# Kernel tuning notes

Measured on AMD Instinct MI355X. Metric: run time of the kernel, lower is better.

## Reference

```python
import jax, jax.numpy as jnp
import numpy as np

# Default widths from CWT.__init__: round((exp(linspace(0,2.5,5))-1)*30)+1
WIDTHS = [1, 27, 76, 167, 336]


def _morlet_int_psi():
    """pywt 'morl' wavelet: psi(t)=exp(-t^2/2)*cos(5t) on [-8,8], precision=10,
    integrated (cumulative) as in pywt.integrate_wavelet."""
    precision = 10
    n = 2 ** precision
    lb, ub = -8.0, 8.0
    t = np.linspace(lb, ub, n)
    psi = np.exp(-t ** 2 / 2.0) * np.cos(5.0 * t)
    step = t[1] - t[0]
    int_psi = np.cumsum(psi) * step
    return int_psi, step, lb, ub, n


def _filters(widths):
    """Per-scale resampled integrated wavelet, as in pywt.cwt.
    pywt uses np.convolve(data, int_psi[j][::-1]) (which flips its kernel);
    lax conv is a correlation (no flip), so the equivalent lax kernel is int_psi[j]."""
    int_psi, step, lb, ub, n = _morlet_int_psi()
    filts = []
    for scale in widths:
        j = (np.arange(scale * (ub - lb) + 1) / (scale * step)).astype(np.int64)
        j = j[j < n]
        filts.append(int_psi[j].astype(np.float32))
    return filts

_FILTERS = _filters(WIDTHS)


def _cwt_forward(x):
    # x: [N, T, C]; conv along T, channels independent
    N, T, C = x.shape
    xt = x.transpose(0, 2, 1).reshape(N * C, 1, T)  # [N*C, 1, T]
    outs = []
    for scale, f in zip(WIDTHS, _FILTERS):
        L = f.shape[0]
        k = jnp.asarray(f)[None, None, :]  # [out=1, in=1, L]
        # 'full' convolution: pad L-1 on each side
        conv = jax.lax.conv_general_dilated(xt, k, window_strides=(1,), padding=[(L - 1, L - 1)])  # [N*C,1,T+L-1]
        coef = (-np.sqrt(float(scale))) * jnp.diff(conv, axis=-1)  # [N*C,1,T+L-2]
        d = (coef.shape[-1] - T) / 2.0  # trim to central T samples (pywt)
        lo = int(np.floor(d))
        hi = coef.shape[-1] - int(np.ceil(d))
        coef = coef[..., lo:hi]  # [N*C, 1, T]
        outs.append(coef.reshape(N, C, T))
    out = jnp.stack(outs, axis=0)  # [F, N, C, T]
    return out.transpose(1, 3, 2, 0)  # [N, T, C, F]


def setup_inputs() -> dict:
    key = jax.random.key(0)
    x = jax.random.normal(key, (16, 2048, 64), dtype=jnp.float32)
    return {"x": x}


def reference(x):
    return _cwt_forward(x)
```

## Files before the change

kernel.cpp:

```cpp
#include <hip/hip_runtime.h>
#include <hip/hip_fp16.h>
#include <math.h>

#define NB    16
#define T     2048
#define NC    64
#define NROWS (NB*NC)
#define PADL2 2696
#define XSH_N 7440

#define WTOT_U4 19840

#define WS_XT    (1u<<19)
#define WS_OUTT  ((1u<<19) + (1u<<22))

typedef _Float16 half8  __attribute__((ext_vector_type(8)));
typedef _Float16 half4v __attribute__((ext_vector_type(4)));
typedef float    f32x4  __attribute__((ext_vector_type(4)));

__global__ __launch_bounds__(1024) void cwt_prep(const float* __restrict__ x,
                                                 __half* __restrict__ xT,
                                                 __half* __restrict__ W) {
    __shared__ double ps[1024];
    __shared__ double sc[1024];
    __shared__ float  k32[1024];
    __shared__ float  tile4[4][64 * 65];
    const int tid = threadIdx.x;

    if (blockIdx.x == 0) {
        uint4* W4 = (uint4*)W;
        const uint4 z = make_uint4(0u, 0u, 0u, 0u);
        for (int i = tid; i < WTOT_U4; i += 1024) W4[i] = z;

        const double delta = 16.0 / 1023.0;
        double t = (tid == 1023) ? 8.0 : (-8.0 + delta * (double)tid);
        ps[tid] = exp(-0.5 * t * t) * cos(5.0 * t);
        __syncthreads();

        double* a = ps; double* b = sc;
        for (int off = 1; off < 1024; off <<= 1) {
            double v = a[tid];
            if (tid >= off) v += a[tid - off];
            b[tid] = v;
            __syncthreads();
            double* tmp = a; a = b; b = tmp;
        }
        const double step = ((-8.0 + delta) + 8.0);
        k32[tid] = (float)(a[tid] * step);
        __syncthreads();

        constexpr int SCe[5]   = {336, 167, 76, 27, 1};
        constexpr int KS2[5]   = {5408, 2720, 1248, 480, 64};
        constexpr int WOFFe[5] = {0, 86528, 130048, 150016, 157696};
        constexpr int CLOe[5]  = {0, 42, 65, 77, 83};
        for (int sl = 0; sl < 5; ++sl) {
            const int s = SCe[sl];
            const int L = 16 * s + 1;
            const double c = (double)s * step;
            const float sq = (float)sqrt((double)s);
            const int posoff = PADL2 - 8 * s - 1;
            const int kb0 = posoff - 32 * CLOe[sl];
            __half* wb = W + WOFFe[sl];
            const int Ks = KS2[sl];
            for (int i = tid; i <= L; i += 1024) {
                float g; bool wr = true;
                if (i == 0) {
                    g = sq * k32[0];
                } else if (i == L) {
                    long long jl = (long long)((double)(L - 1) / c);
                    if (jl > 1023) jl = 1023;
                    g = -sq * k32[jl];
                } else {
                    long long j1 = (long long)((double)i / c);
                    long long j0 = (long long)((double)(i - 1) / c);
                    if (j1 > 1023) j1 = 1023;
                    if (j0 > 1023) j0 = 1023;
                    wr = (j1 > j0);
                    g = sq * (k32[j1] - k32[j0]);
                }
                if (wr) {
                    const __half hg = __float2half(g);
                    const int kb = kb0 + i;
                    #pragma unroll
                    for (int bb = 0; bb < 16; ++bb)
                        wb[bb * Ks + kb + bb] = hg;
                }
            }
        }
    } else {
        const int g    = tid >> 8;
        const int t256 = tid & 255;
        const int ti   = (blockIdx.x - 1) * 4 + g;
        const int n    = ti >> 5;
        const int t0   = (ti & 31) << 6;
        float* tl = tile4[g];

        const float4* src = (const float4*)(x + ((size_t)(n * T + t0)) * NC);
        #pragma unroll
        for (int k = 0; k < 4; ++k) {
            float4 v = src[t256 + 256 * k];
            const int flat = (t256 + 256 * k) * 4;
            const int tt = flat >> 6, c = flat & 63;
            tl[tt * 65 + c + 0] = v.x;
            tl[tt * 65 + c + 1] = v.y;
            tl[tt * 65 + c + 2] = v.z;
            tl[tt * 65 + c + 3] = v.w;
        }
        __syncthreads();
        const int lane = t256 & 63, w4 = t256 >> 6;
        for (int cc = w4; cc < 64; cc += 4) {
            xT[((size_t)(n * 64 + cc)) * T + t0 + lane] = __float2half(tl[lane * 65 + cc]);
        }
    }
}

template<int N, int DEPTH>
__device__ __forceinline__ void conv_seg(int c0, int c1,
                                         const _Float16* __restrict__ xb,
                                         const _Float16* const (&ap)[5],
                                         f32x4 (&acc)[5][4]) {
    half8 A[DEPTH][N];
    half8 B[DEPTH][4];
    #pragma unroll
    for (int d = 0; d < DEPTH; ++d) {
        const int ko = (c0 + d) << 5;
        #pragma unroll
        for (int sl = 0; sl < N; ++sl) A[d][sl] = *(const half8*)(ap[sl] + ko);
        #pragma unroll
        for (int j = 0; j < 4; ++j)   B[d][j]  = *(const half8*)(xb + 256 * j + ko);
    }
    int c = c0;
    for (; c + DEPTH <= c1; c += DEPTH) {
        #pragma unroll
        for (int d = 0; d < DEPTH; ++d) {
            #pragma unroll
            for (int sl = 0; sl < N; ++sl) {
                acc[sl][0] = __builtin_amdgcn_mfma_f32_16x16x32_f16(A[d][sl], B[d][0], acc[sl][0], 0, 0, 0);
                acc[sl][1] = __builtin_amdgcn_mfma_f32_16x16x32_f16(A[d][sl], B[d][1], acc[sl][1], 0, 0, 0);
                acc[sl][2] = __builtin_amdgcn_mfma_f32_16x16x32_f16(A[d][sl], B[d][2], acc[sl][2], 0, 0, 0);
                acc[sl][3] = __builtin_amdgcn_mfma_f32_16x16x32_f16(A[d][sl], B[d][3], acc[sl][3], 0, 0, 0);
            }
            const int ko = (c + DEPTH + d) << 5;
            #pragma unroll
            for (int sl = 0; sl < N; ++sl) A[d][sl] = *(const half8*)(ap[sl] + ko);
            #pragma unroll
            for (int j = 0; j < 4; ++j)   B[d][j]  = *(const half8*)(xb + 256 * j + ko);
        }
    }
    #pragma unroll
    for (int d = 0; d < DEPTH; ++d) {
        if (d < c1 - c) {
            #pragma unroll
            for (int sl = 0; sl < N; ++sl) {
                acc[sl][0] = __builtin_amdgcn_mfma_f32_16x16x32_f16(A[d][sl], B[d][0], acc[sl][0], 0, 0, 0);
                acc[sl][1] = __builtin_amdgcn_mfma_f32_16x16x32_f16(A[d][sl], B[d][1], acc[sl][1], 0, 0, 0);
                acc[sl][2] = __builtin_amdgcn_mfma_f32_16x16x32_f16(A[d][sl], B[d][2], acc[sl][2], 0, 0, 0);
                acc[sl][3] = __builtin_amdgcn_mfma_f32_16x16x32_f16(A[d][sl], B[d][3], acc[sl][3], 0, 0, 0);
            }
        }
    }
}

__global__ __launch_bounds__(128, 2) void cwt_conv_mfma(const __half* __restrict__ xT,
                                                        const __half* __restrict__ Wg,
                                                        __half* __restrict__ outT) {
    constexpr int KS2[5]   = {5408, 2720, 1248, 480, 64};
    constexpr int WOFFe[5] = {0, 86528, 130048, 150016, 157696};
    constexpr int CLOe[5]  = {0, 42, 65, 77, 83};
    constexpr int OS[5]    = {4, 3, 2, 1, 0};

    __shared__ _Float16 xsh[XSH_N];
    __shared__ _Float16 ostage[2048];
    const int tid  = threadIdx.x;
    const int row  = blockIdx.x;
    const int nidx = row >> 6;
    const int cidx = row & 63;
    const int lane = tid & 63;
    const int w    = tid >> 6;
    const int mcol = lane & 15;
    const int grp  = lane >> 4;

    {
        uint4* x4 = (uint4*)xsh;
        const uint4 z = make_uint4(0u, 0u, 0u, 0u);
        for (int i = tid; i < XSH_N / 8; i += 128)
            if (i < PADL2 / 8 || i >= (PADL2 + T) / 8) x4[i] = z;
        const uint4* src = (const uint4*)(xT + (size_t)row * T);
        x4[PADL2 / 8 + tid] = src[tid];
        x4[PADL2 / 8 + 128 + tid] = src[128 + tid];
    }
    __syncthreads();

    const _Float16* xb = xsh + 1024 * w + 16 * mcol + 8 * grp;
    const _Float16* ap[5];
    #pragma unroll
    for (int sl = 0; sl < 5; ++sl)
        ap[sl] = (const _Float16*)Wg + WOFFe[sl] + mcol * KS2[sl] + 8 * grp
                 - (CLOe[sl] << 5);

    f32x4 acc[5][4];
    #pragma unroll
    for (int sl = 0; sl < 5; ++sl)
        #pragma unroll
        for (int j = 0; j < 4; ++j)
            acc[sl][j] = (f32x4){0.f, 0.f, 0.f, 0.f};

    conv_seg<1,3>(  0,  42, xb, ap, acc);
    conv_seg<2,3>( 42,  65, xb, ap, acc);
    conv_seg<3,2>( 65,  77, xb, ap, acc);
    conv_seg<4,2>( 77,  83, xb, ap, acc);
    conv_seg<5,2>( 83,  85, xb, ap, acc);
    conv_seg<4,2>( 85,  92, xb, ap, acc);
    conv_seg<3,2>( 92, 104, xb, ap, acc);
    conv_seg<2,3>(104, 127, xb, ap, acc);
    conv_seg<1,3>(127, 169, xb, ap, acc);

    _Float16* os = ostage + 1024 * w;
    #pragma unroll
    for (int sl = 0; sl < 5; ++sl) {
        #pragma unroll
        for (int j = 0; j < 4; ++j) {
            half4v h;
            #pragma unroll
            for (int r = 0; r < 4; ++r) h[r] = (_Float16)acc[sl][j][r];
            *(half4v*)(os + 256 * j + 16 * mcol + 4 * grp) = h;
        }
        half8 o0 = *(const half8*)(os + 16 * lane);
        half8 o1 = *(const half8*)(os + 16 * lane + 8);
        __half* ob = outT + ((size_t)(((nidx * 128 + 64 * w + lane) * 64 + cidx) * 5 + OS[sl])) * 16;
        *(half8*)(ob)     = o0;
        *(half8*)(ob + 8) = o1;
    }
}

__global__ __launch_bounds__(256) void cwt_fix(const __half* __restrict__ outT,
                                               float* __restrict__ out) {
    __shared__ float tile[16 * 320];
    const int b  = blockIdx.x;
    const int n  = b >> 7;
    const int tb = b & 127;
    const int tid = threadIdx.x;

    const uint4* src = (const uint4*)(outT + (size_t)(n * 128 + tb) * 5120);
    for (int i = tid; i < 640; i += 256) {
        uint4 v = src[i];
        const __half* h = (const __half*)&v;
        const int h0  = i * 8;
        const int sg  = h0 >> 4;
        const int tt0 = h0 & 15;
        #pragma unroll
        for (int k = 0; k < 8; ++k) tile[(tt0 + k) * 320 + sg] = __half2float(h[k]);
    }
    __syncthreads();
    float4* dst = (float4*)(out + (size_t)(n * 2048 + tb * 16) * 320);
    const float4* tl = (const float4*)tile;
    for (int k = tid; k < 1280; k += 256) dst[k] = tl[k];
}

extern "C" void kernel_launch(void* const* d_in, const int* in_sizes, int n_in,
                              void* d_out, int out_size, void* d_ws, size_t ws_size,
                              hipStream_t stream) {
    const float* x = (const float*)d_in[0];
    float* out = (float*)d_out;
    char* ws = (char*)d_ws;

    __half* W    = (__half*)ws;
    __half* xT   = (__half*)(ws + WS_XT);
    __half* outT = (__half*)(ws + WS_OUTT);

    cwt_prep<<<129, 1024, 0, stream>>>(x, xT, W);
    cwt_conv_mfma<<<NROWS, 128, 0, stream>>>(xT, W, outT);
    cwt_fix<<<2048, 256, 0, stream>>>(outT, out);
}
```

Baseline: 144.0 us.

## Split conv reduction across wave pairs and parallelize filter build over 16 blocks

The MFMA conv kernel now runs 4 waves per block instead of 2. Each pair of waves handles half of the K-segment range for the same output tile, and the partial accumulators are reduced through shared memory before the write-out. The prep kernel's single filter-building block becomes 16 blocks, one per diagonal shift, each zeroing and writing its own slice of the Toeplitz weight matrix. The goal is more parallelism and latency hiding in the conv and less serial work in prep, at the cost of extra LDS usage, two reduction barriers and redundant cumsum work in each prep block.

```diff
diff --git a/kernel.cpp b/kernel.cpp
--- a/kernel.cpp
+++ b/kernel.cpp
@@ -9,7 +9,6 @@
 #define PADL2 2696
 #define XSH_N 7440
 
-#define WTOT_U4 19840
 
 #define WS_XT    (1u<<19)
 #define WS_OUTT  ((1u<<19) + (1u<<22))
@@ -27,10 +26,22 @@
     __shared__ float  tile4[4][64 * 65];
     const int tid = threadIdx.x;
 
-    if (blockIdx.x == 0) {
-        uint4* W4 = (uint4*)W;
-        const uint4 z = make_uint4(0u, 0u, 0u, 0u);
-        for (int i = tid; i < WTOT_U4; i += 1024) W4[i] = z;
+    if (blockIdx.x < 16) {
+        const int bb = blockIdx.x;
+        constexpr int SCe[5]   = {336, 167, 76, 27, 1};
+        constexpr int KS2[5]   = {5408, 2720, 1248, 480, 64};
+        constexpr int WOFFe[5] = {0, 86528, 130048, 150016, 157696};
+        constexpr int CLOe[5]  = {0, 42, 65, 77, 83};
+
+        {
+            const uint4 z = make_uint4(0u, 0u, 0u, 0u);
+            #pragma unroll
+            for (int sl = 0; sl < 5; ++sl) {
+                uint4* z4 = (uint4*)(W + WOFFe[sl] + bb * KS2[sl]);
+                const int n8 = KS2[sl] / 8;
+                for (int i = tid; i < n8; i += 1024) z4[i] = z;
+            }
+        }
 
         const double delta = 16.0 / 1023.0;
         double t = (tid == 1023) ? 8.0 : (-8.0 + delta * (double)tid);
@@ -49,10 +60,6 @@
         k32[tid] = (float)(a[tid] * step);
         __syncthreads();
 
-        constexpr int SCe[5]   = {336, 167, 76, 27, 1};
-        constexpr int KS2[5]   = {5408, 2720, 1248, 480, 64};
-        constexpr int WOFFe[5] = {0, 86528, 130048, 150016, 157696};
-        constexpr int CLOe[5]  = {0, 42, 65, 77, 83};
         for (int sl = 0; sl < 5; ++sl) {
             const int s = SCe[sl];
             const int L = 16 * s + 1;
@@ -79,18 +86,14 @@
                     g = sq * (k32[j1] - k32[j0]);
                 }
                 if (wr) {
-                    const __half hg = __float2half(g);
-                    const int kb = kb0 + i;
-                    #pragma unroll
-                    for (int bb = 0; bb < 16; ++bb)
-                        wb[bb * Ks + kb + bb] = hg;
+                    wb[bb * Ks + kb0 + i + bb] = __float2half(g);
                 }
             }
         }
     } else {
         const int g    = tid >> 8;
         const int t256 = tid & 255;
-        const int ti   = (blockIdx.x - 1) * 4 + g;
+        const int ti   = (blockIdx.x - 16) * 4 + g;
         const int n    = ti >> 5;
         const int t0   = (ti & 31) << 6;
         float* tl = tile4[g];
@@ -161,7 +164,7 @@
     }
 }
 
-__global__ __launch_bounds__(128, 2) void cwt_conv_mfma(const __half* __restrict__ xT,
+__global__ __launch_bounds__(256, 4) void cwt_conv_mfma(const __half* __restrict__ xT,
                                                         const __half* __restrict__ Wg,
                                                         __half* __restrict__ outT) {
     constexpr int KS2[5]   = {5408, 2720, 1248, 480, 64};
@@ -171,27 +174,29 @@
 
     __shared__ _Float16 xsh[XSH_N];
     __shared__ _Float16 ostage[2048];
+    __shared__ float    red[2][2][1088];
     const int tid  = threadIdx.x;
     const int row  = blockIdx.x;
     const int nidx = row >> 6;
     const int cidx = row & 63;
     const int lane = tid & 63;
     const int w    = tid >> 6;
+    const int wh   = w & 1;
+    const int wp   = w >> 1;
     const int mcol = lane & 15;
     const int grp  = lane >> 4;
 
     {
         uint4* x4 = (uint4*)xsh;
         const uint4 z = make_uint4(0u, 0u, 0u, 0u);
-        for (int i = tid; i < XSH_N / 8; i += 128)
+        for (int i = tid; i < XSH_N / 8; i += 256)
             if (i < PADL2 / 8 || i >= (PADL2 + T) / 8) x4[i] = z;
         const uint4* src = (const uint4*)(xT + (size_t)row * T);
         x4[PADL2 / 8 + tid] = src[tid];
-        x4[PADL2 / 8 + 128 + tid] = src[128 + tid];
     }
     __syncthreads();
 
-    const _Float16* xb = xsh + 1024 * w + 16 * mcol + 8 * grp;
+    const _Float16* xb = xsh + 1024 * wh + 16 * mcol + 8 * grp;
     const _Float16* ap[5];
     #pragma unroll
     for (int sl = 0; sl < 5; ++sl)
@@ -205,31 +210,61 @@
         for (int j = 0; j < 4; ++j)
             acc[sl][j] = (f32x4){0.f, 0.f, 0.f, 0.f};
 
-    conv_seg<1,3>(  0,  42, xb, ap, acc);
-    conv_seg<2,3>( 42,  65, xb, ap, acc);
-    conv_seg<3,2>( 65,  77, xb, ap, acc);
-    conv_seg<4,2>( 77,  83, xb, ap, acc);
-    conv_seg<5,2>( 83,  85, xb, ap, acc);
-    conv_seg<4,2>( 85,  92, xb, ap, acc);
-    conv_seg<3,2>( 92, 104, xb, ap, acc);
-    conv_seg<2,3>(104, 127, xb, ap, acc);
-    conv_seg<1,3>(127, 169, xb, ap, acc);
-
-    _Float16* os = ostage + 1024 * w;
-    #pragma unroll
-    for (int sl = 0; sl < 5; ++sl) {
-        #pragma unroll
-        for (int j = 0; j < 4; ++j) {
-            half4v h;
-            #pragma unroll
-            for (int r = 0; r < 4; ++r) h[r] = (_Float16)acc[sl][j][r];
-            *(half4v*)(os + 256 * j + 16 * mcol + 4 * grp) = h;
-        }
-        half8 o0 = *(const half8*)(os + 16 * lane);
-        half8 o1 = *(const half8*)(os + 16 * lane + 8);
-        __half* ob = outT + ((size_t)(((nidx * 128 + 64 * w + lane) * 64 + cidx) * 5 + OS[sl])) * 16;
-        *(half8*)(ob)     = o0;
-        *(half8*)(ob + 8) = o1;
+    if (wp == 0) {
+        conv_seg<1,3>(  0,  42, xb, ap, acc);
+        conv_seg<2,3>( 42,  65, xb, ap, acc);
+        conv_seg<3,2>( 65,  77, xb, ap, acc);
+        conv_seg<4,2>( 77,  83, xb, ap, acc);
+        conv_seg<5,2>( 83,  85, xb, ap, acc);
+    } else {
+        conv_seg<4,2>( 85,  92, xb, ap, acc);
+        conv_seg<3,2>( 92, 104, xb, ap, acc);
+        conv_seg<2,3>(104, 127, xb, ap, acc);
+        conv_seg<1,3>(127, 169, xb, ap, acc);
+    }
+
+    #pragma unroll
+    for (int rnd = 0; rnd < 2; ++rnd) {
+        const int s0 = rnd * 2;
+        if (wp == 1) {
+            #pragma unroll
+            for (int s = 0; s < 2; ++s)
+                #pragma unroll
+                for (int j = 0; j < 4; ++j)
+                    #pragma unroll
+                    for (int r = 0; r < 4; ++r)
+                        red[s][wh][lane * 17 + j * 4 + r] = acc[s0 + s][j][r];
+        }
+        __syncthreads();
+        if (wp == 0) {
+            #pragma unroll
+            for (int s = 0; s < 2; ++s)
+                #pragma unroll
+                for (int j = 0; j < 4; ++j)
+                    #pragma unroll
+                    for (int r = 0; r < 4; ++r)
+                        acc[s0 + s][j][r] += red[s][wh][lane * 17 + j * 4 + r];
+        }
+        __syncthreads();
+    }
+
+    if (wp == 0) {
+        _Float16* os = ostage + 1024 * wh;
+        #pragma unroll
+        for (int sl = 0; sl < 5; ++sl) {
+            #pragma unroll
+            for (int j = 0; j < 4; ++j) {
+                half4v h;
+                #pragma unroll
+                for (int r = 0; r < 4; ++r) h[r] = (_Float16)acc[sl][j][r];
+                *(half4v*)(os + 256 * j + 16 * mcol + 4 * grp) = h;
+            }
+            half8 o0 = *(const half8*)(os + 16 * lane);
+            half8 o1 = *(const half8*)(os + 16 * lane + 8);
+            __half* ob = outT + ((size_t)(((nidx * 128 + 64 * wh + lane) * 64 + cidx) * 5 + OS[sl])) * 16;
+            *(half8*)(ob)     = o0;
+            *(half8*)(ob + 8) = o1;
+        }
     }
 }
 
@@ -268,7 +303,7 @@
     __half* xT   = (__half*)(ws + WS_XT);
     __half* outT = (__half*)(ws + WS_OUTT);
 
-    cwt_prep<<<129, 1024, 0, stream>>>(x, xT, W);
-    cwt_conv_mfma<<<NROWS, 128, 0, stream>>>(xT, W, outT);
+    cwt_prep<<<144, 1024, 0, stream>>>(x, xT, W);
+    cwt_conv_mfma<<<NROWS, 256, 0, stream>>>(xT, W, outT);
     cwt_fix<<<2048, 256, 0, stream>>>(outT, out);
 }
```

Measured after the change: 210.9 us. 1.46x slower.

## Split conv rows across two blocks and parallelize filter build over 16 blocks

Applied to the files above, without the earlier changes.

The convolution kernel now launches two blocks per signal row. Each block computes half the time tiles, with accumulators halved from [5][4] to [5][2] and launch bounds raised to 4 blocks per SM, which gives more parallelism and occupancy. Each block still loads the full row into shared memory, so the shared staging work is duplicated. The prep kernel spreads zeroing and filter construction over 16 blocks (one per diagonal shift) instead of one, at the cost of recomputing the wavelet prefix scan in each block.

```diff
diff --git a/kernel.cpp b/kernel.cpp
--- a/kernel.cpp
+++ b/kernel.cpp
@@ -9,7 +9,6 @@
 #define PADL2 2696
 #define XSH_N 7440
 
-#define WTOT_U4 19840
 
 #define WS_XT    (1u<<19)
 #define WS_OUTT  ((1u<<19) + (1u<<22))
@@ -27,10 +26,22 @@
     __shared__ float  tile4[4][64 * 65];
     const int tid = threadIdx.x;
 
-    if (blockIdx.x == 0) {
-        uint4* W4 = (uint4*)W;
-        const uint4 z = make_uint4(0u, 0u, 0u, 0u);
-        for (int i = tid; i < WTOT_U4; i += 1024) W4[i] = z;
+    if (blockIdx.x < 16) {
+        const int bb = blockIdx.x;
+        constexpr int SCe[5]   = {336, 167, 76, 27, 1};
+        constexpr int KS2[5]   = {5408, 2720, 1248, 480, 64};
+        constexpr int WOFFe[5] = {0, 86528, 130048, 150016, 157696};
+        constexpr int CLOe[5]  = {0, 42, 65, 77, 83};
+
+        {
+            const uint4 z = make_uint4(0u, 0u, 0u, 0u);
+            #pragma unroll
+            for (int sl = 0; sl < 5; ++sl) {
+                uint4* z4 = (uint4*)(W + WOFFe[sl] + bb * KS2[sl]);
+                const int n8 = KS2[sl] / 8;
+                for (int i = tid; i < n8; i += 1024) z4[i] = z;
+            }
+        }
 
         const double delta = 16.0 / 1023.0;
         double t = (tid == 1023) ? 8.0 : (-8.0 + delta * (double)tid);
@@ -49,10 +60,6 @@
         k32[tid] = (float)(a[tid] * step);
         __syncthreads();
 
-        constexpr int SCe[5]   = {336, 167, 76, 27, 1};
-        constexpr int KS2[5]   = {5408, 2720, 1248, 480, 64};
-        constexpr int WOFFe[5] = {0, 86528, 130048, 150016, 157696};
-        constexpr int CLOe[5]  = {0, 42, 65, 77, 83};
         for (int sl = 0; sl < 5; ++sl) {
             const int s = SCe[sl];
             const int L = 16 * s + 1;
@@ -79,18 +86,14 @@
                     g = sq * (k32[j1] - k32[j0]);
                 }
                 if (wr) {
-                    const __half hg = __float2half(g);
-                    const int kb = kb0 + i;
-                    #pragma unroll
-                    for (int bb = 0; bb < 16; ++bb)
-                        wb[bb * Ks + kb + bb] = hg;
+                    wb[bb * Ks + kb0 + i + bb] = __float2half(g);
                 }
             }
         }
     } else {
         const int g    = tid >> 8;
         const int t256 = tid & 255;
-        const int ti   = (blockIdx.x - 1) * 4 + g;
+        const int ti   = (blockIdx.x - 16) * 4 + g;
         const int n    = ti >> 5;
         const int t0   = (ti & 31) << 6;
         float* tl = tile4[g];
@@ -118,16 +121,16 @@
 __device__ __forceinline__ void conv_seg(int c0, int c1,
                                          const _Float16* __restrict__ xb,
                                          const _Float16* const (&ap)[5],
-                                         f32x4 (&acc)[5][4]) {
+                                         f32x4 (&acc)[5][2]) {
     half8 A[DEPTH][N];
-    half8 B[DEPTH][4];
+    half8 B[DEPTH][2];
     #pragma unroll
     for (int d = 0; d < DEPTH; ++d) {
         const int ko = (c0 + d) << 5;
         #pragma unroll
         for (int sl = 0; sl < N; ++sl) A[d][sl] = *(const half8*)(ap[sl] + ko);
         #pragma unroll
-        for (int j = 0; j < 4; ++j)   B[d][j]  = *(const half8*)(xb + 256 * j + ko);
+        for (int j = 0; j < 2; ++j)   B[d][j]  = *(const half8*)(xb + 256 * j + ko);
     }
     int c = c0;
     for (; c + DEPTH <= c1; c += DEPTH) {
@@ -137,14 +140,12 @@
             for (int sl = 0; sl < N; ++sl) {
                 acc[sl][0] = __builtin_amdgcn_mfma_f32_16x16x32_f16(A[d][sl], B[d][0], acc[sl][0], 0, 0, 0);
                 acc[sl][1] = __builtin_amdgcn_mfma_f32_16x16x32_f16(A[d][sl], B[d][1], acc[sl][1], 0, 0, 0);
-                acc[sl][2] = __builtin_amdgcn_mfma_f32_16x16x32_f16(A[d][sl], B[d][2], acc[sl][2], 0, 0, 0);
-                acc[sl][3] = __builtin_amdgcn_mfma_f32_16x16x32_f16(A[d][sl], B[d][3], acc[sl][3], 0, 0, 0);
             }
             const int ko = (c + DEPTH + d) << 5;
             #pragma unroll
             for (int sl = 0; sl < N; ++sl) A[d][sl] = *(const half8*)(ap[sl] + ko);
             #pragma unroll
-            for (int j = 0; j < 4; ++j)   B[d][j]  = *(const half8*)(xb + 256 * j + ko);
+            for (int j = 0; j < 2; ++j)   B[d][j]  = *(const half8*)(xb + 256 * j + ko);
         }
     }
     #pragma unroll
@@ -154,14 +155,12 @@
             for (int sl = 0; sl < N; ++sl) {
                 acc[sl][0] = __builtin_amdgcn_mfma_f32_16x16x32_f16(A[d][sl], B[d][0], acc[sl][0], 0, 0, 0);
                 acc[sl][1] = __builtin_amdgcn_mfma_f32_16x16x32_f16(A[d][sl], B[d][1], acc[sl][1], 0, 0, 0);
-                acc[sl][2] = __builtin_amdgcn_mfma_f32_16x16x32_f16(A[d][sl], B[d][2], acc[sl][2], 0, 0, 0);
-                acc[sl][3] = __builtin_amdgcn_mfma_f32_16x16x32_f16(A[d][sl], B[d][3], acc[sl][3], 0, 0, 0);
-            }
-        }
-    }
-}
-
-__global__ __launch_bounds__(128, 2) void cwt_conv_mfma(const __half* __restrict__ xT,
+            }
+        }
+    }
+}
+
+__global__ __launch_bounds__(128, 4) void cwt_conv_mfma(const __half* __restrict__ xT,
                                                         const __half* __restrict__ Wg,
                                                         __half* __restrict__ outT) {
     constexpr int KS2[5]   = {5408, 2720, 1248, 480, 64};
@@ -170,9 +169,11 @@
     constexpr int OS[5]    = {4, 3, 2, 1, 0};
 
     __shared__ _Float16 xsh[XSH_N];
-    __shared__ _Float16 ostage[2048];
+    __shared__ _Float16 ostage[1024];
     const int tid  = threadIdx.x;
-    const int row  = blockIdx.x;
+    const int bid  = blockIdx.x;
+    const int row  = bid >> 1;
+    const int h    = bid & 1;
     const int nidx = row >> 6;
     const int cidx = row & 63;
     const int lane = tid & 63;
@@ -191,18 +192,19 @@
     }
     __syncthreads();
 
-    const _Float16* xb = xsh + 1024 * w + 16 * mcol + 8 * grp;
+    const int g0 = 64 * h + 32 * w;
+    const _Float16* xb = xsh + 16 * g0 + 16 * mcol + 8 * grp;
     const _Float16* ap[5];
     #pragma unroll
     for (int sl = 0; sl < 5; ++sl)
         ap[sl] = (const _Float16*)Wg + WOFFe[sl] + mcol * KS2[sl] + 8 * grp
                  - (CLOe[sl] << 5);
 
-    f32x4 acc[5][4];
+    f32x4 acc[5][2];
     #pragma unroll
     for (int sl = 0; sl < 5; ++sl)
         #pragma unroll
-        for (int j = 0; j < 4; ++j)
+        for (int j = 0; j < 2; ++j)
             acc[sl][j] = (f32x4){0.f, 0.f, 0.f, 0.f};
 
     conv_seg<1,3>(  0,  42, xb, ap, acc);
@@ -215,21 +217,21 @@
     conv_seg<2,3>(104, 127, xb, ap, acc);
     conv_seg<1,3>(127, 169, xb, ap, acc);
 
-    _Float16* os = ostage + 1024 * w;
+    _Float16* os = ostage + 512 * w;
     #pragma unroll
     for (int sl = 0; sl < 5; ++sl) {
         #pragma unroll
-        for (int j = 0; j < 4; ++j) {
-            half4v h;
-            #pragma unroll
-            for (int r = 0; r < 4; ++r) h[r] = (_Float16)acc[sl][j][r];
-            *(half4v*)(os + 256 * j + 16 * mcol + 4 * grp) = h;
-        }
-        half8 o0 = *(const half8*)(os + 16 * lane);
-        half8 o1 = *(const half8*)(os + 16 * lane + 8);
-        __half* ob = outT + ((size_t)(((nidx * 128 + 64 * w + lane) * 64 + cidx) * 5 + OS[sl])) * 16;
-        *(half8*)(ob)     = o0;
-        *(half8*)(ob + 8) = o1;
+        for (int j = 0; j < 2; ++j) {
+            half4v hv;
+            #pragma unroll
+            for (int r = 0; r < 4; ++r) hv[r] = (_Float16)acc[sl][j][r];
+            *(half4v*)(os + 256 * j + 16 * mcol + 4 * grp) = hv;
+        }
+        half8 o = *(const half8*)(os + 8 * lane);
+        const int tb = g0 + (lane >> 1);
+        __half* ob = outT + ((size_t)(((nidx * 128 + tb) * 64 + cidx) * 5 + OS[sl])) * 16
+                     + 8 * (lane & 1);
+        *(half8*)(ob) = o;
     }
 }
 
@@ -268,7 +270,7 @@
     __half* xT   = (__half*)(ws + WS_XT);
     __half* outT = (__half*)(ws + WS_OUTT);
 
-    cwt_prep<<<129, 1024, 0, stream>>>(x, xT, W);
-    cwt_conv_mfma<<<NROWS, 128, 0, stream>>>(xT, W, outT);
+    cwt_prep<<<144, 1024, 0, stream>>>(x, xT, W);
+    cwt_conv_mfma<<<2 * NROWS, 128, 0, stream>>>(xT, W, outT);
     cwt_fix<<<2048, 256, 0, stream>>>(outT, out);
 }
```

Result: slower. 192.8 us (+33.9%).

## Switch Toeplitz conv to 32x32x16 MFMA and parallelize filter build over 32 blocks

Applied to the files above, without the earlier changes.

Replaces the 16x16x32 MFMA tiling (four accumulators per scale) with one 32x32x16 MFMA per scale. This cuts B-operand loads per wave and lengthens each instruction, in exchange for twice as many K steps. The banded Toeplitz weight matrices are rebuilt with 32 shifted rows, and their construction is spread across 32 prep blocks instead of one serial block. Wavelet evaluation now uses float expf/cosf, which can slightly change the filter values.

```diff
diff --git a/kernel.cpp b/kernel.cpp
--- a/kernel.cpp
+++ b/kernel.cpp
@@ -8,15 +8,15 @@
 #define NROWS (NB*NC)
 #define PADL2 2696
 #define XSH_N 7440
-
-#define WTOT_U4 19840
-
-#define WS_XT    (1u<<19)
-#define WS_OUTT  ((1u<<19) + (1u<<22))
+#define XSH_PAD 7568
+
+
+#define WS_XT    655360u
+#define WS_OUTT  4849664u
 
 typedef _Float16 half8  __attribute__((ext_vector_type(8)));
 typedef _Float16 half4v __attribute__((ext_vector_type(4)));
-typedef float    f32x4  __attribute__((ext_vector_type(4)));
+typedef float    f32x16 __attribute__((ext_vector_type(16)));
 
 __global__ __launch_bounds__(1024) void cwt_prep(const float* __restrict__ x,
                                                  __half* __restrict__ xT,
@@ -27,14 +27,29 @@
     __shared__ float  tile4[4][64 * 65];
     const int tid = threadIdx.x;
 
-    if (blockIdx.x == 0) {
-        uint4* W4 = (uint4*)W;
-        const uint4 z = make_uint4(0u, 0u, 0u, 0u);
-        for (int i = tid; i < WTOT_U4; i += 1024) W4[i] = z;
+    if (blockIdx.x < 32) {
+        const int bb = blockIdx.x;
+        constexpr int SCe[5]    = {336, 167, 76, 27, 1};
+        constexpr int KS16[5]   = {5424, 2720, 1264, 480, 64};
+        constexpr int WOFF32[5] = {0, 173568, 260608, 301056, 316416};
+        constexpr int CLO16[5]  = {0, 84, 130, 154, 167};
+
+        {
+            const uint4 z = make_uint4(0u, 0u, 0u, 0u);
+            #pragma unroll
+            for (int sl = 0; sl < 5; ++sl) {
+                uint4* z4 = (uint4*)(W + WOFF32[sl] + bb * KS16[sl]);
+                const int n8 = KS16[sl] / 8;
+                for (int i = tid; i < n8; i += 1024) z4[i] = z;
+            }
+        }
 
         const double delta = 16.0 / 1023.0;
         double t = (tid == 1023) ? 8.0 : (-8.0 + delta * (double)tid);
-        ps[tid] = exp(-0.5 * t * t) * cos(5.0 * t);
+        {
+            const float tf = (float)t;
+            ps[tid] = (double)(expf(-0.5f * tf * tf) * cosf(5.0f * tf));
+        }
         __syncthreads();
 
         double* a = ps; double* b = sc;
@@ -49,19 +64,14 @@
         k32[tid] = (float)(a[tid] * step);
         __syncthreads();
 
-        constexpr int SCe[5]   = {336, 167, 76, 27, 1};
-        constexpr int KS2[5]   = {5408, 2720, 1248, 480, 64};
-        constexpr int WOFFe[5] = {0, 86528, 130048, 150016, 157696};
-        constexpr int CLOe[5]  = {0, 42, 65, 77, 83};
         for (int sl = 0; sl < 5; ++sl) {
             const int s = SCe[sl];
             const int L = 16 * s + 1;
             const double c = (double)s * step;
             const float sq = (float)sqrt((double)s);
             const int posoff = PADL2 - 8 * s - 1;
-            const int kb0 = posoff - 32 * CLOe[sl];
-            __half* wb = W + WOFFe[sl];
-            const int Ks = KS2[sl];
+            const int kb0 = posoff - 16 * CLO16[sl];
+            __half* wb = W + WOFF32[sl] + bb * KS16[sl];
             for (int i = tid; i <= L; i += 1024) {
                 float g; bool wr = true;
                 if (i == 0) {
@@ -79,18 +89,14 @@
                     g = sq * (k32[j1] - k32[j0]);
                 }
                 if (wr) {
-                    const __half hg = __float2half(g);
-                    const int kb = kb0 + i;
-                    #pragma unroll
-                    for (int bb = 0; bb < 16; ++bb)
-                        wb[bb * Ks + kb + bb] = hg;
+                    wb[kb0 + i + bb] = __float2half(g);
                 }
             }
         }
     } else {
         const int g    = tid >> 8;
         const int t256 = tid & 255;
-        const int ti   = (blockIdx.x - 1) * 4 + g;
+        const int ti   = (blockIdx.x - 32) * 4 + g;
         const int n    = ti >> 5;
         const int t0   = (ti & 31) << 6;
         float* tl = tile4[g];
@@ -118,45 +124,35 @@
 __device__ __forceinline__ void conv_seg(int c0, int c1,
                                          const _Float16* __restrict__ xb,
                                          const _Float16* const (&ap)[5],
-                                         f32x4 (&acc)[5][4]) {
+                                         f32x16 (&acc)[5]) {
     half8 A[DEPTH][N];
-    half8 B[DEPTH][4];
+    half8 B[DEPTH];
     #pragma unroll
     for (int d = 0; d < DEPTH; ++d) {
-        const int ko = (c0 + d) << 5;
+        const int ko = (c0 + d) << 4;
         #pragma unroll
         for (int sl = 0; sl < N; ++sl) A[d][sl] = *(const half8*)(ap[sl] + ko);
-        #pragma unroll
-        for (int j = 0; j < 4; ++j)   B[d][j]  = *(const half8*)(xb + 256 * j + ko);
+        B[d] = *(const half8*)(xb + ko);
     }
     int c = c0;
     for (; c + DEPTH <= c1; c += DEPTH) {
         #pragma unroll
         for (int d = 0; d < DEPTH; ++d) {
             #pragma unroll
-            for (int sl = 0; sl < N; ++sl) {
-                acc[sl][0] = __builtin_amdgcn_mfma_f32_16x16x32_f16(A[d][sl], B[d][0], acc[sl][0], 0, 0, 0);
-                acc[sl][1] = __builtin_amdgcn_mfma_f32_16x16x32_f16(A[d][sl], B[d][1], acc[sl][1], 0, 0, 0);
-                acc[sl][2] = __builtin_amdgcn_mfma_f32_16x16x32_f16(A[d][sl], B[d][2], acc[sl][2], 0, 0, 0);
-                acc[sl][3] = __builtin_amdgcn_mfma_f32_16x16x32_f16(A[d][sl], B[d][3], acc[sl][3], 0, 0, 0);
-            }
-            const int ko = (c + DEPTH + d) << 5;
+            for (int sl = 0; sl < N; ++sl)
+                acc[sl] = __builtin_amdgcn_mfma_f32_32x32x16_f16(A[d][sl], B[d], acc[sl], 0, 0, 0);
+            const int ko = (c + DEPTH + d) << 4;
             #pragma unroll
             for (int sl = 0; sl < N; ++sl) A[d][sl] = *(const half8*)(ap[sl] + ko);
-            #pragma unroll
-            for (int j = 0; j < 4; ++j)   B[d][j]  = *(const half8*)(xb + 256 * j + ko);
+            B[d] = *(const half8*)(xb + ko);
         }
     }
     #pragma unroll
     for (int d = 0; d < DEPTH; ++d) {
         if (d < c1 - c) {
             #pragma unroll
-            for (int sl = 0; sl < N; ++sl) {
-                acc[sl][0] = __builtin_amdgcn_mfma_f32_16x16x32_f16(A[d][sl], B[d][0], acc[sl][0], 0, 0, 0);
-                acc[sl][1] = __builtin_amdgcn_mfma_f32_16x16x32_f16(A[d][sl], B[d][1], acc[sl][1], 0, 0, 0);
-                acc[sl][2] = __builtin_amdgcn_mfma_f32_16x16x32_f16(A[d][sl], B[d][2], acc[sl][2], 0, 0, 0);
-                acc[sl][3] = __builtin_amdgcn_mfma_f32_16x16x32_f16(A[d][sl], B[d][3], acc[sl][3], 0, 0, 0);
-            }
+            for (int sl = 0; sl < N; ++sl)
+                acc[sl] = __builtin_amdgcn_mfma_f32_32x32x16_f16(A[d][sl], B[d], acc[sl], 0, 0, 0);
         }
     }
 }
@@ -164,12 +160,12 @@
 __global__ __launch_bounds__(128, 2) void cwt_conv_mfma(const __half* __restrict__ xT,
                                                         const __half* __restrict__ Wg,
                                                         __half* __restrict__ outT) {
-    constexpr int KS2[5]   = {5408, 2720, 1248, 480, 64};
-    constexpr int WOFFe[5] = {0, 86528, 130048, 150016, 157696};
-    constexpr int CLOe[5]  = {0, 42, 65, 77, 83};
-    constexpr int OS[5]    = {4, 3, 2, 1, 0};
-
-    __shared__ _Float16 xsh[XSH_N];
+    constexpr int KS16[5]   = {5424, 2720, 1264, 480, 64};
+    constexpr int WOFF32[5] = {0, 173568, 260608, 301056, 316416};
+    constexpr int CLO16[5]  = {0, 84, 130, 154, 167};
+    constexpr int OS[5]     = {4, 3, 2, 1, 0};
+
+    __shared__ _Float16 xsh[XSH_PAD];
     __shared__ _Float16 ostage[2048];
     const int tid  = threadIdx.x;
     const int row  = blockIdx.x;
@@ -177,8 +173,8 @@
     const int cidx = row & 63;
     const int lane = tid & 63;
     const int w    = tid >> 6;
-    const int mcol = lane & 15;
-    const int grp  = lane >> 4;
+    const int col  = lane & 31;
+    const int kh   = lane >> 5;
 
     {
         uint4* x4 = (uint4*)xsh;
@@ -191,39 +187,38 @@
     }
     __syncthreads();
 
-    const _Float16* xb = xsh + 1024 * w + 16 * mcol + 8 * grp;
+    const _Float16* xb = xsh + 32 * (32 * w + col) + 8 * kh;
     const _Float16* ap[5];
     #pragma unroll
     for (int sl = 0; sl < 5; ++sl)
-        ap[sl] = (const _Float16*)Wg + WOFFe[sl] + mcol * KS2[sl] + 8 * grp
-                 - (CLOe[sl] << 5);
-
-    f32x4 acc[5][4];
+        ap[sl] = (const _Float16*)Wg + WOFF32[sl] + col * KS16[sl] + 8 * kh
+                 - 16 * CLO16[sl];
+
+    f32x16 acc[5];
     #pragma unroll
     for (int sl = 0; sl < 5; ++sl)
         #pragma unroll
-        for (int j = 0; j < 4; ++j)
-            acc[sl][j] = (f32x4){0.f, 0.f, 0.f, 0.f};
-
-    conv_seg<1,3>(  0,  42, xb, ap, acc);
-    conv_seg<2,3>( 42,  65, xb, ap, acc);
-    conv_seg<3,2>( 65,  77, xb, ap, acc);
-    conv_seg<4,2>( 77,  83, xb, ap, acc);
-    conv_seg<5,2>( 83,  85, xb, ap, acc);
-    conv_seg<4,2>( 85,  92, xb, ap, acc);
-    conv_seg<3,2>( 92, 104, xb, ap, acc);
-    conv_seg<2,3>(104, 127, xb, ap, acc);
-    conv_seg<1,3>(127, 169, xb, ap, acc);
+        for (int r = 0; r < 16; ++r) acc[sl][r] = 0.f;
+
+    conv_seg<1,4>(  0,  84, xb, ap, acc);
+    conv_seg<2,3>( 84, 130, xb, ap, acc);
+    conv_seg<3,2>(130, 154, xb, ap, acc);
+    conv_seg<4,2>(154, 167, xb, ap, acc);
+    conv_seg<5,1>(167, 171, xb, ap, acc);
+    conv_seg<4,2>(171, 184, xb, ap, acc);
+    conv_seg<3,2>(184, 209, xb, ap, acc);
+    conv_seg<2,3>(209, 254, xb, ap, acc);
+    conv_seg<1,4>(254, 339, xb, ap, acc);
 
     _Float16* os = ostage + 1024 * w;
     #pragma unroll
     for (int sl = 0; sl < 5; ++sl) {
         #pragma unroll
-        for (int j = 0; j < 4; ++j) {
-            half4v h;
-            #pragma unroll
-            for (int r = 0; r < 4; ++r) h[r] = (_Float16)acc[sl][j][r];
-            *(half4v*)(os + 256 * j + 16 * mcol + 4 * grp) = h;
+        for (int rq = 0; rq < 4; ++rq) {
+            half4v hv;
+            #pragma unroll
+            for (int r = 0; r < 4; ++r) hv[r] = (_Float16)acc[sl][4 * rq + r];
+            *(half4v*)(os + 32 * col + 8 * rq + 4 * kh) = hv;
         }
         half8 o0 = *(const half8*)(os + 16 * lane);
         half8 o1 = *(const half8*)(os + 16 * lane + 8);
@@ -268,7 +263,7 @@
     __half* xT   = (__half*)(ws + WS_XT);
     __half* outT = (__half*)(ws + WS_OUTT);
 
-    cwt_prep<<<129, 1024, 0, stream>>>(x, xT, W);
+    cwt_prep<<<160, 1024, 0, stream>>>(x, xT, W);
     cwt_conv_mfma<<<NROWS, 128, 0, stream>>>(xT, W, outT);
     cwt_fix<<<2048, 256, 0, stream>>>(outT, out);
 }
```

After: 190.4 us. 32.2% more time.
